# Optimization experiments

Measured on AMD Instinct MI355X. Metric: run time of the kernel, lower is better.

The kernel has to match this reference:

```python
import jax, jax.numpy as jnp
import numpy as np

D_IN = 2048
D_OUT = 2048
NUM_HEADS = 16
HEAD_DIM = D_OUT // NUM_HEADS


def setup_inputs() -> dict:
    key = jax.random.key(0)
    k_x, k_qkv, k_proj, k_b = jax.random.split(key, 4)
    x = jax.random.normal(k_x, (2, 2048, D_IN), dtype=jnp.float32)
    # torch Linear(d_in, 3*d_out, bias=False): weight [3*d_out, d_in]; store transposed [d_in, 3*d_out]
    Wqkv = jax.random.normal(k_qkv, (D_IN, 3 * D_OUT), dtype=jnp.float32) / np.sqrt(D_IN)
    Wproj = jax.random.normal(k_proj, (D_OUT, D_OUT), dtype=jnp.float32) / np.sqrt(D_OUT)
    bproj = jax.random.normal(k_b, (D_OUT,), dtype=jnp.float32) * 0.01
    return {"x": x, "Wqkv": Wqkv, "Wproj": Wproj, "bproj": bproj}


def reference(x, Wqkv, Wproj, bproj):
    B, S, _ = x.shape
    qkv = x @ Wqkv  # [B, S, 3*D_OUT]
    qkv = qkv.reshape(B, S, 3, NUM_HEADS, HEAD_DIM)
    qkv = jnp.transpose(qkv, (2, 0, 3, 1, 4))  # [3, B, H, S, Dh]
    q, k, v = qkv[0], qkv[1], qkv[2]
    scale = 1.0 / np.sqrt(HEAD_DIM).astype(np.float32)
    scores = jnp.einsum('bhqd,bhkd->bhqk', q, k) * scale  # [B, H, S, S]
    causal = jnp.tril(jnp.ones((S, S), dtype=bool))
    scores = jnp.where(causal, scores, jnp.finfo(scores.dtype).min)
    attn = jax.nn.softmax(scores, axis=-1)
    out = jnp.einsum('bhqk,bhkd->bhqd', attn, v)  # [B, H, S, Dh]
    out = jnp.transpose(out, (0, 2, 1, 3)).reshape(B, S, D_OUT)
    return out @ Wproj + bproj
```

## Files before the change

### kernel.cpp

```cpp
#include <hip/hip_runtime.h>
#include <stdint.h>

typedef __attribute__((ext_vector_type(8))) short short8;
typedef __attribute__((ext_vector_type(4))) float f32x4;
typedef __attribute__((ext_vector_type(16))) float f32x16;
typedef __attribute__((ext_vector_type(4))) unsigned short u16x4;

typedef unsigned short u16;

constexpr int S_LEN = 2048;
constexpr int DH    = 128;

__device__ __forceinline__ u16 f2bf(float f) {
    union { float f; unsigned u; } v; v.f = f;
    unsigned r = v.u + 0x7FFFu + ((v.u >> 16) & 1u);
    return (u16)(r >> 16);
}
__device__ __forceinline__ void gl_lds16(const void* g, void* l) {
    __builtin_amdgcn_global_load_lds((const __attribute__((address_space(1))) void*)g,
                                     (__attribute__((address_space(3))) void*)l,
                                     16, 0, 0);
}

__global__ __launch_bounds__(256) void convx(const float* __restrict__ src,
                                             u16* __restrict__ dst) {
    size_t i = ((size_t)blockIdx.x * 256 + threadIdx.x) * 8;
    f32x4 a = *(const f32x4*)(src + i);
    f32x4 b = *(const f32x4*)(src + i + 4);
    short8 r;
    r[0] = (short)f2bf(a[0]); r[1] = (short)f2bf(a[1]);
    r[2] = (short)f2bf(a[2]); r[3] = (short)f2bf(a[3]);
    r[4] = (short)f2bf(b[0]); r[5] = (short)f2bf(b[1]);
    r[6] = (short)f2bf(b[2]); r[7] = (short)f2bf(b[3]);
    *(short8*)(dst + i) = r;
}

__global__ void convT(const float* __restrict__ src, u16* __restrict__ dst,
                      int rows, int cols) {
    __shared__ u16 tile[32][33];
    int c0 = blockIdx.x * 32, r0 = blockIdx.y * 32;
    int tx = threadIdx.x, ty = threadIdx.y;
#pragma unroll
    for (int i = 0; i < 32; i += 8)
        tile[ty + i][tx] = f2bf(src[(size_t)(r0 + ty + i) * cols + c0 + tx]);
    __syncthreads();
#pragma unroll
    for (int i = 0; i < 32; i += 8)
        dst[(size_t)(c0 + ty + i) * rows + r0 + tx] = tile[tx][ty + i];
}

__global__ __launch_bounds__(512, 2) void gemm_qkv(
        const u16* __restrict__ A, const u16* __restrict__ BT,
        u16* __restrict__ Qo, u16* __restrict__ Ko, u16* __restrict__ VTo) {
    __shared__ __align__(16) u16 lA[2][256 * 64];
    __shared__ __align__(16) u16 lB[2][256 * 64];
    const int tid = threadIdx.x;
    const int lane = tid & 63, wave = tid >> 6;
    const int quad = lane >> 4, l16 = lane & 15;
    const int wr = wave >> 2, wc = wave & 3;
    const int m0 = blockIdx.y * 256, n0 = blockIdx.x * 256;
    const int sw = l16 & 7;
    const int c4 = tid & 7;
    const int rih0 = tid >> 3;
    f32x4 acc[8][4] = {};

    auto stageA = [&](int h, int t1, int nb) {
#pragma unroll
        for (int j = 0; j < 2; ++j) {
            int rih = j * 64 + rih0;
            int row = (rih & 63) + h * 64 + (rih >> 6) * 128;
            gl_lds16(A + (size_t)(m0 + row) * 2048 + t1 * 64 + ((c4 ^ (row & 7)) * 8),
                     &lA[nb][row * 64 + c4 * 8]);
        }
    };
    auto stageB = [&](int h, int t1, int nb) {
#pragma unroll
        for (int j = 0; j < 2; ++j) {
            int rih = j * 64 + rih0;
            int row = (rih & 31) + h * 32 + (rih >> 5) * 64;
            gl_lds16(BT + (size_t)(n0 + row) * 2048 + t1 * 64 + ((c4 ^ (row & 7)) * 8),
                     &lB[nb][row * 64 + c4 * 8]);
        }
    };

    stageA(0, 0, 0); stageB(0, 0, 0); stageA(1, 0, 0); stageB(1, 0, 0);
    asm volatile("s_waitcnt vmcnt(4)\n\ts_barrier" ::: "memory");

    constexpr int NT = 32;
    for (int t = 0; t < NT; ++t) {
        const int buf = t & 1, nb = buf ^ 1;
        const bool pf = (t + 1 < NT);
#pragma unroll
        for (int ph = 0; ph < 4; ++ph) {
            const int qm = ph & 1, qn = ph >> 1;
            short8 af[4][2], bfr[2][2];
            const int abase = (wr * 128 + qm * 64 + l16) * 64;
            const int bbase = (wc * 64 + qn * 32 + l16) * 64;
#pragma unroll
            for (int m = 0; m < 4; ++m)
#pragma unroll
                for (int ks = 0; ks < 2; ++ks)
                    af[m][ks] = *(const short8*)&lA[buf][abase + m * 1024 + (((ks * 4 + quad) ^ sw)) * 8];
#pragma unroll
            for (int n = 0; n < 2; ++n)
#pragma unroll
                for (int ks = 0; ks < 2; ++ks)
                    bfr[n][ks] = *(const short8*)&lB[buf][bbase + n * 1024 + (((ks * 4 + quad) ^ sw)) * 8];
            if (pf) {
                if      (ph == 0) stageA(0, t + 1, nb);
                else if (ph == 1) stageB(0, t + 1, nb);
                else if (ph == 2) stageA(1, t + 1, nb);
                else              stageB(1, t + 1, nb);
            }
            __builtin_amdgcn_s_setprio(1);
#pragma unroll
            for (int m = 0; m < 4; ++m)
#pragma unroll
                for (int n = 0; n < 2; ++n)
#pragma unroll
                    for (int ks = 0; ks < 2; ++ks)
                        acc[qm * 4 + m][qn * 2 + n] = __builtin_amdgcn_mfma_f32_16x16x32_bf16(
                            af[m][ks], bfr[n][ks], acc[qm * 4 + m][qn * 2 + n], 0, 0, 0);
            __builtin_amdgcn_s_setprio(0);
            if (pf)             asm volatile("s_waitcnt vmcnt(4)\n\ts_barrier" ::: "memory");
            else if (ph == 0)   asm volatile("s_waitcnt vmcnt(2)\n\ts_barrier" ::: "memory");
            else                asm volatile("s_waitcnt vmcnt(0)\n\ts_barrier" ::: "memory");
        }
    }

#pragma unroll
    for (int m8 = 0; m8 < 8; ++m8) {
        int r0r = m0 + wr * 128 + m8 * 16 + quad * 4;
        int b = r0r >> 11, s0 = r0r & 2047;
#pragma unroll
        for (int n4 = 0; n4 < 4; ++n4) {
            int cc = n0 + wc * 64 + n4 * 16 + l16;
            int which = cc >> 11, hd = (cc >> 7) & 15, dh = cc & 127;
            if (which < 2) {
                u16* dst = which == 0 ? Qo : Ko;
#pragma unroll
                for (int rg = 0; rg < 4; ++rg)
                    dst[(size_t)((b * 16 + hd) * 2048 + s0 + rg) * 128 + dh] = f2bf(acc[m8][n4][rg]);
            } else {
                u16x4 v;
#pragma unroll
                for (int rg = 0; rg < 4; ++rg) v[rg] = f2bf(acc[m8][n4][rg]);
                *(u16x4*)&VTo[((size_t)(b * 16 + hd) * 128 + dh) * 2048 + s0] = v;
            }
        }
    }
}

__global__ __launch_bounds__(256, 2) void attn_kern(
        u16* __restrict__ QOp, const u16* __restrict__ Kp,
        const u16* __restrict__ VTp) {
    __shared__ __align__(16) u16 lK[2][64 * 128];
    __shared__ __align__(16) u16 lV[2][128 * 64];
    const int tid = threadIdx.x, lane = tid & 63, wave = tid >> 6;
    const int ql = lane & 31, hi = lane >> 5;
    const int qb = (blockIdx.y < 8) ? (15 - (int)blockIdx.y) : ((int)blockIdx.y - 8);
    const int bh = blockIdx.x;
    const int qbase = qb * 128 + wave * 32;
    const int qmax = qbase + 31;
    const int nkt = 2 * qb + 2;
    u16* Qh = QOp + (size_t)bh * S_LEN * DH;
    const u16* Kh = Kp + (size_t)bh * S_LEN * DH;
    const u16* VTh = VTp + (size_t)bh * DH * S_LEN;

    short8 qf[8];
#pragma unroll
    for (int c = 0; c < 8; ++c)
        qf[c] = *(const short8*)&Qh[(size_t)(qbase + ql) * 128 + c * 16 + hi * 8];

    f32x16 acc[4] = {};
    float mrun = -1e30f, lrun = 0.f;
    const float SC = 0.08838834764831845f * 1.44269504088896f;

    auto stage = [&](int kt, int b) {
        const u16* ks = Kh + (size_t)kt * 64 * 128;
#pragma unroll
        for (int p = 0; p < 4; ++p) {
            int slot = p * 256 + tid;
            int row = slot >> 4, c4 = slot & 15;
            gl_lds16(ks + row * 128 + ((c4 ^ (row & 15)) * 8), &lK[b][slot * 8]);
        }
        const u16* vs = VTh + kt * 64;
#pragma unroll
        for (int p = 0; p < 4; ++p) {
            int slot = p * 256 + tid;
            int row = slot >> 3, c4 = slot & 7;
            gl_lds16(vs + (size_t)row * 2048 + ((c4 ^ (row & 7)) * 8), &lV[b][slot * 8]);
        }
    };

    stage(0, 0);
    __syncthreads();

    for (int kt = 0; kt < nkt; ++kt) {
        const int buf = kt & 1;
        if (kt + 1 < nkt) stage(kt + 1, buf ^ 1);
        if (kt * 64 <= qmax) {
            const bool part = (kt * 64 + 63 > qbase);
            f32x16 s0 = {}, s1 = {};
            __builtin_amdgcn_s_setprio(1);
#pragma unroll
            for (int c = 0; c < 8; ++c) {
                int sl = ((c * 2 + hi) ^ (ql & 15)) * 8;
                short8 k0 = *(const short8*)&lK[buf][ql * 128 + sl];
                short8 k1 = *(const short8*)&lK[buf][(32 + ql) * 128 + sl];
                s0 = __builtin_amdgcn_mfma_f32_32x32x16_bf16(k0, qf[c], s0, 0, 0, 0);
                s1 = __builtin_amdgcn_mfma_f32_32x32x16_bf16(k1, qf[c], s1, 0, 0, 0);
            }
            __builtin_amdgcn_s_setprio(0);
            float pv0[16], pv1[16];
            float pm = -1e30f;
            const int qg = qbase + ql;
#pragma unroll
            for (int r = 0; r < 16; ++r) {
                int krow = (r & 3) + 8 * (r >> 2) + 4 * hi;
                float a = s0[r] * SC;
                float b = s1[r] * SC;
                if (part) {
                    if (kt * 64 + krow > qg)      a = -1e30f;
                    if (kt * 64 + 32 + krow > qg) b = -1e30f;
                }
                pv0[r] = a; pv1[r] = b;
                pm = fmaxf(pm, fmaxf(a, b));
            }
            pm = fmaxf(pm, __shfl_xor(pm, 32));
            if (__any(pm - mrun > 8.f)) {
                float mn = fmaxf(mrun, pm);
                float al = exp2f(mrun - mn);
                mrun = mn;
                lrun *= al;
#pragma unroll
                for (int r = 0; r < 16; ++r) {
                    float ar = __shfl(al, (r & 3) + 8 * (r >> 2) + 4 * hi);
#pragma unroll
                    for (int dc = 0; dc < 4; ++dc)
                        acc[dc][r] *= ar;
                }
            }
            float rs = 0.f;
#pragma unroll
            for (int r = 0; r < 16; ++r) {
                pv0[r] = exp2f(pv0[r] - mrun);
                pv1[r] = exp2f(pv1[r] - mrun);
                rs += pv0[r] + pv1[r];
            }
            rs += __shfl_xor(rs, 32);
            lrun += rs;
            unsigned X0[8], X1[8];
#pragma unroll
            for (int i = 0; i < 8; ++i) {
                X0[i] = (unsigned)f2bf(pv0[2 * i]) | ((unsigned)f2bf(pv0[2 * i + 1]) << 16);
                X1[i] = (unsigned)f2bf(pv1[2 * i]) | ((unsigned)f2bf(pv1[2 * i + 1]) << 16);
            }
            short8 pa[4];
#pragma unroll
            for (int t = 0; t < 2; ++t)
#pragma unroll
                for (int h = 0; h < 2; ++h) {
                    unsigned x0 = t ? X1[4 * h + 0] : X0[4 * h + 0];
                    unsigned x1 = t ? X1[4 * h + 1] : X0[4 * h + 1];
                    unsigned x2 = t ? X1[4 * h + 2] : X0[4 * h + 2];
                    unsigned x3 = t ? X1[4 * h + 3] : X0[4 * h + 3];
                    unsigned sx0 = (unsigned)__shfl_xor((int)x0, 32);
                    unsigned sx1 = (unsigned)__shfl_xor((int)x1, 32);
                    unsigned sx2 = (unsigned)__shfl_xor((int)x2, 32);
                    unsigned sx3 = (unsigned)__shfl_xor((int)x3, 32);
                    union { unsigned u[4]; short8 s; } uf;
                    uf.u[0] = hi ? sx2 : x0;
                    uf.u[1] = hi ? sx3 : x1;
                    uf.u[2] = hi ? x2 : sx0;
                    uf.u[3] = hi ? x3 : sx1;
                    pa[t * 2 + h] = uf.s;
                }
            __builtin_amdgcn_s_setprio(1);
#pragma unroll
            for (int dc = 0; dc < 4; ++dc) {
                const int rv = dc * 32 + ql;
#pragma unroll
                for (int kc = 0; kc < 4; ++kc) {
                    short8 vf = *(const short8*)&lV[buf][rv * 64 + (((kc * 2 + hi) ^ (ql & 7)) * 8)];
                    acc[dc] = __builtin_amdgcn_mfma_f32_32x32x16_bf16(pa[kc], vf, acc[dc], 0, 0, 0);
                }
            }
            __builtin_amdgcn_s_setprio(0);
        }
        __syncthreads();
    }

    float linv = 1.f / lrun;
#pragma unroll
    for (int r = 0; r < 16; ++r) {
        int qr = (r & 3) + 8 * (r >> 2) + 4 * hi;
        float lr = __shfl(linv, qr);
        int qq = qbase + qr;
#pragma unroll
        for (int dc = 0; dc < 4; ++dc)
            Qh[(size_t)qq * 128 + dc * 32 + ql] = f2bf(acc[dc][r] * lr);
    }
}

__global__ __launch_bounds__(256) void gemm_proj(
        const u16* __restrict__ QO, const u16* __restrict__ BT,
        const float* __restrict__ bias, float* __restrict__ out) {
    __shared__ __align__(16) u16 lA[128 * 32];
    __shared__ __align__(16) u16 lB[128 * 32];
    const int tid = threadIdx.x;
    const int lane = tid & 63, wave = tid >> 6;
    const int quad = lane >> 4, l16 = lane & 15;
    const int wm = wave >> 1, wn = wave & 1;
    const int m0 = blockIdx.y * 128, n0 = blockIdx.x * 128;
    f32x4 acc[4][4] = {};
    const int rbase = tid >> 2;
    const int cofs  = (tid & 3) * 8;

    for (int k0 = 0; k0 < 2048; k0 += 32) {
#pragma unroll
        for (int it = 0; it < 2; ++it) {
            int row = m0 + it * 64 + rbase;
            int b = row >> 11, s = row & 2047;
            int k = k0 + cofs, h = k >> 7, dh = k & 127;
            gl_lds16(QO + ((size_t)(b * 16 + h) * 2048 + s) * 128 + dh, &lA[(it * 256 + tid) * 8]);
            gl_lds16(BT + (size_t)(n0 + it * 64 + rbase) * 2048 + k0 + cofs, &lB[(it * 256 + tid) * 8]);
        }
        __syncthreads();
        short8 af[4], bf[4];
#pragma unroll
        for (int i = 0; i < 4; ++i) {
            af[i] = *(const short8*)&lA[(wm * 64 + i * 16 + l16) * 32 + quad * 8];
            bf[i] = *(const short8*)&lB[(wn * 64 + i * 16 + l16) * 32 + quad * 8];
        }
#pragma unroll
        for (int im = 0; im < 4; ++im)
#pragma unroll
            for (int in = 0; in < 4; ++in)
                acc[im][in] = __builtin_amdgcn_mfma_f32_16x16x32_bf16(af[im], bf[in], acc[im][in], 0, 0, 0);
        __syncthreads();
    }
#pragma unroll
    for (int im = 0; im < 4; ++im) {
        int r0r = m0 + wm * 64 + im * 16 + quad * 4;
#pragma unroll
        for (int in = 0; in < 4; ++in) {
            int cc = n0 + wn * 64 + in * 16 + l16;
            float bv = bias[cc];
#pragma unroll
            for (int rg = 0; rg < 4; ++rg)
                out[(size_t)(r0r + rg) * 2048 + cc] = acc[im][in][rg] + bv;
        }
    }
}

extern "C" void kernel_launch(void* const* d_in, const int* in_sizes, int n_in,
                              void* d_out, int out_size, void* d_ws, size_t ws_size,
                              hipStream_t stream) {
    const float *x = nullptr, *Wqkv = nullptr, *Wproj = nullptr, *bproj = nullptr;
    for (int i = 0; i < n_in; ++i) {
        int sz = in_sizes[i];
        if      (sz == 2 * 2048 * 2048) x     = (const float*)d_in[i];
        else if (sz == 2048 * 6144)     Wqkv  = (const float*)d_in[i];
        else if (sz == 2048 * 2048)     Wproj = (const float*)d_in[i];
        else if (sz == 2048)            bproj = (const float*)d_in[i];
    }
    float* out = (float*)d_out;

    u16* xb     = (u16*)d_ws;
    u16* WqkvT  = xb    + (size_t)4096 * 2048;
    u16* Qb     = WqkvT + (size_t)6144 * 2048;
    u16* Kb     = Qb    + (size_t)32 * 2048 * 128;
    u16* VTb    = Kb    + (size_t)32 * 2048 * 128;
    u16* WprojT = xb;

    convx<<<dim3(4096), dim3(256), 0, stream>>>(x, xb);
    convT<<<dim3(192, 64), dim3(32, 8), 0, stream>>>(Wqkv, WqkvT, 2048, 6144);
    gemm_qkv<<<dim3(24, 16), dim3(512), 0, stream>>>(xb, WqkvT, Qb, Kb, VTb);
    convT<<<dim3(64, 64), dim3(32, 8), 0, stream>>>(Wproj, WprojT, 2048, 2048);
    attn_kern<<<dim3(32, 16), dim3(256), 0, stream>>>(Qb, Kb, VTb);
    gemm_proj<<<dim3(16, 32), dim3(256), 0, stream>>>(Qb, WprojT, bproj, out);
}
```

Baseline: 428.4 us.

## Shrink QKV GEMM tile to 128x256 and restructure into two-phase pipeline

The QKV projection GEMM block tile drops from 256x256 to 128x256, which doubles the grid to 768 workgroups and halves the A-tile LDS buffer and per-thread accumulators. The inner K loop changes from four quarter-phases to two halves, each with its own wait/barrier and prefetch of the next tile. The goal is better occupancy and load balance across CUs, with fewer registers. The cost is lower arithmetic intensity per block, so more global and L2 traffic for B.

```diff
diff --git a/kernel.cpp b/kernel.cpp
--- a/kernel.cpp
+++ b/kernel.cpp
@@ -52,23 +52,22 @@
 __global__ __launch_bounds__(512, 2) void gemm_qkv(
         const u16* __restrict__ A, const u16* __restrict__ BT,
         u16* __restrict__ Qo, u16* __restrict__ Ko, u16* __restrict__ VTo) {
-    __shared__ __align__(16) u16 lA[2][256 * 64];
+    __shared__ __align__(16) u16 lA[2][128 * 64];
     __shared__ __align__(16) u16 lB[2][256 * 64];
     const int tid = threadIdx.x;
     const int lane = tid & 63, wave = tid >> 6;
     const int quad = lane >> 4, l16 = lane & 15;
     const int wr = wave >> 2, wc = wave & 3;
-    const int m0 = blockIdx.y * 256, n0 = blockIdx.x * 256;
+    const int m0 = blockIdx.y * 128, n0 = blockIdx.x * 256;
     const int sw = l16 & 7;
     const int c4 = tid & 7;
-    const int rih0 = tid >> 3;
-    f32x4 acc[8][4] = {};
-
-    auto stageA = [&](int h, int t1, int nb) {
+    f32x4 acc[4][4] = {};
+
+    auto stageA = [&](int t1, int nb) {
 #pragma unroll
         for (int j = 0; j < 2; ++j) {
-            int rih = j * 64 + rih0;
-            int row = (rih & 63) + h * 64 + (rih >> 6) * 128;
+            int idx = j * 512 + tid;
+            int row = idx >> 3;
             gl_lds16(A + (size_t)(m0 + row) * 2048 + t1 * 64 + ((c4 ^ (row & 7)) * 8),
                      &lA[nb][row * 64 + c4 * 8]);
         }
@@ -76,75 +75,82 @@
     auto stageB = [&](int h, int t1, int nb) {
 #pragma unroll
         for (int j = 0; j < 2; ++j) {
-            int rih = j * 64 + rih0;
+            int rih = (j * 512 + tid) >> 3;
             int row = (rih & 31) + h * 32 + (rih >> 5) * 64;
             gl_lds16(BT + (size_t)(n0 + row) * 2048 + t1 * 64 + ((c4 ^ (row & 7)) * 8),
                      &lB[nb][row * 64 + c4 * 8]);
         }
     };
 
-    stageA(0, 0, 0); stageB(0, 0, 0); stageA(1, 0, 0); stageB(1, 0, 0);
-    asm volatile("s_waitcnt vmcnt(4)\n\ts_barrier" ::: "memory");
+    stageA(0, 0); stageB(0, 0, 0); stageB(1, 0, 0);
 
     constexpr int NT = 32;
     for (int t = 0; t < NT; ++t) {
         const int buf = t & 1, nb = buf ^ 1;
         const bool pf = (t + 1 < NT);
-#pragma unroll
-        for (int ph = 0; ph < 4; ++ph) {
-            const int qm = ph & 1, qn = ph >> 1;
-            short8 af[4][2], bfr[2][2];
-            const int abase = (wr * 128 + qm * 64 + l16) * 64;
-            const int bbase = (wc * 64 + qn * 32 + l16) * 64;
-#pragma unroll
-            for (int m = 0; m < 4; ++m)
+        asm volatile("s_waitcnt vmcnt(2)\n\ts_barrier" ::: "memory");
+        short8 af[4][2], bf0[2][2];
+        const int abase = (wr * 64 + l16) * 64;
+        const int bbase = (wc * 64 + l16) * 64;
+#pragma unroll
+        for (int m = 0; m < 4; ++m)
+#pragma unroll
+            for (int ks = 0; ks < 2; ++ks)
+                af[m][ks] = *(const short8*)&lA[buf][abase + m * 1024 + (((ks * 4 + quad) ^ sw)) * 8];
+#pragma unroll
+        for (int n = 0; n < 2; ++n)
+#pragma unroll
+            for (int ks = 0; ks < 2; ++ks)
+                bf0[n][ks] = *(const short8*)&lB[buf][bbase + n * 1024 + (((ks * 4 + quad) ^ sw)) * 8];
+        if (pf) { stageA(t + 1, nb); stageB(0, t + 1, nb); }
+        __builtin_amdgcn_s_setprio(1);
+#pragma unroll
+        for (int m = 0; m < 4; ++m)
+#pragma unroll
+            for (int n = 0; n < 2; ++n)
 #pragma unroll
                 for (int ks = 0; ks < 2; ++ks)
-                    af[m][ks] = *(const short8*)&lA[buf][abase + m * 1024 + (((ks * 4 + quad) ^ sw)) * 8];
+                    acc[m][n] = __builtin_amdgcn_mfma_f32_16x16x32_bf16(
+                        af[m][ks], bf0[n][ks], acc[m][n], 0, 0, 0);
+        __builtin_amdgcn_s_setprio(0);
+        if (pf) asm volatile("s_waitcnt vmcnt(4)\n\ts_barrier" ::: "memory");
+        else    asm volatile("s_waitcnt vmcnt(0)\n\ts_barrier" ::: "memory");
+        short8 bf1[2][2];
+#pragma unroll
+        for (int n = 0; n < 2; ++n)
+#pragma unroll
+            for (int ks = 0; ks < 2; ++ks)
+                bf1[n][ks] = *(const short8*)&lB[buf][bbase + 2048 + n * 1024 + (((ks * 4 + quad) ^ sw)) * 8];
+        if (pf) stageB(1, t + 1, nb);
+        __builtin_amdgcn_s_setprio(1);
+#pragma unroll
+        for (int m = 0; m < 4; ++m)
 #pragma unroll
             for (int n = 0; n < 2; ++n)
 #pragma unroll
                 for (int ks = 0; ks < 2; ++ks)
-                    bfr[n][ks] = *(const short8*)&lB[buf][bbase + n * 1024 + (((ks * 4 + quad) ^ sw)) * 8];
-            if (pf) {
-                if      (ph == 0) stageA(0, t + 1, nb);
-                else if (ph == 1) stageB(0, t + 1, nb);
-                else if (ph == 2) stageA(1, t + 1, nb);
-                else              stageB(1, t + 1, nb);
-            }
-            __builtin_amdgcn_s_setprio(1);
-#pragma unroll
-            for (int m = 0; m < 4; ++m)
-#pragma unroll
-                for (int n = 0; n < 2; ++n)
-#pragma unroll
-                    for (int ks = 0; ks < 2; ++ks)
-                        acc[qm * 4 + m][qn * 2 + n] = __builtin_amdgcn_mfma_f32_16x16x32_bf16(
-                            af[m][ks], bfr[n][ks], acc[qm * 4 + m][qn * 2 + n], 0, 0, 0);
-            __builtin_amdgcn_s_setprio(0);
-            if (pf)             asm volatile("s_waitcnt vmcnt(4)\n\ts_barrier" ::: "memory");
-            else if (ph == 0)   asm volatile("s_waitcnt vmcnt(2)\n\ts_barrier" ::: "memory");
-            else                asm volatile("s_waitcnt vmcnt(0)\n\ts_barrier" ::: "memory");
-        }
-    }
-
-#pragma unroll
-    for (int m8 = 0; m8 < 8; ++m8) {
-        int r0r = m0 + wr * 128 + m8 * 16 + quad * 4;
+                    acc[m][n + 2] = __builtin_amdgcn_mfma_f32_16x16x32_bf16(
+                        af[m][ks], bf1[n][ks], acc[m][n + 2], 0, 0, 0);
+        __builtin_amdgcn_s_setprio(0);
+    }
+
+#pragma unroll
+    for (int m = 0; m < 4; ++m) {
+        int r0r = m0 + wr * 64 + m * 16 + quad * 4;
         int b = r0r >> 11, s0 = r0r & 2047;
 #pragma unroll
-        for (int n4 = 0; n4 < 4; ++n4) {
-            int cc = n0 + wc * 64 + n4 * 16 + l16;
+        for (int n = 0; n < 4; ++n) {
+            int cc = n0 + wc * 64 + n * 16 + l16;
             int which = cc >> 11, hd = (cc >> 7) & 15, dh = cc & 127;
             if (which < 2) {
                 u16* dst = which == 0 ? Qo : Ko;
 #pragma unroll
                 for (int rg = 0; rg < 4; ++rg)
-                    dst[(size_t)((b * 16 + hd) * 2048 + s0 + rg) * 128 + dh] = f2bf(acc[m8][n4][rg]);
+                    dst[(size_t)((b * 16 + hd) * 2048 + s0 + rg) * 128 + dh] = f2bf(acc[m][n][rg]);
             } else {
                 u16x4 v;
 #pragma unroll
-                for (int rg = 0; rg < 4; ++rg) v[rg] = f2bf(acc[m8][n4][rg]);
+                for (int rg = 0; rg < 4; ++rg) v[rg] = f2bf(acc[m][n][rg]);
                 *(u16x4*)&VTo[((size_t)(b * 16 + hd) * 128 + dh) * 2048 + s0] = v;
             }
         }
@@ -376,7 +382,7 @@
 
     convx<<<dim3(4096), dim3(256), 0, stream>>>(x, xb);
     convT<<<dim3(192, 64), dim3(32, 8), 0, stream>>>(Wqkv, WqkvT, 2048, 6144);
-    gemm_qkv<<<dim3(24, 16), dim3(512), 0, stream>>>(xb, WqkvT, Qb, Kb, VTb);
+    gemm_qkv<<<dim3(24, 32), dim3(512), 0, stream>>>(xb, WqkvT, Qb, Kb, VTb);
     convT<<<dim3(64, 64), dim3(32, 8), 0, stream>>>(Wproj, WprojT, 2048, 2048);
     attn_kern<<<dim3(32, 16), dim3(256), 0, stream>>>(Qb, Kb, VTb);
     gemm_proj<<<dim3(16, 32), dim3(256), 0, stream>>>(Qb, WprojT, bproj, out);
```

Measured after the change: 376.4 us. 1.14x faster.
